# Performance work log

Hardware: AMD Instinct MI355X
Metric: run time of the kernel (lower is better)

The kernel has to match this reference:

```python
import jax, jax.numpy as jnp
import numpy as np
import math

HIDDEN = 1024
NUM_HEADS = 16
HEAD_DIM = 64
NUM_PREV = 4
BATCH = 4
SEQ = 1024
ROPE_BASE = 10000.0


def _rope(x):
    """Apply rotary embedding to x [..., seq, head_dim] (rotate-half form)."""
    d = x.shape[-1]
    s = x.shape[-2]
    inv_freq = 1.0 / (ROPE_BASE ** (jnp.arange(0, d, 2, dtype=jnp.float32) / d))
    ang = jnp.arange(s, dtype=jnp.float32)[:, None] * inv_freq[None, :]  # [s, d/2]
    cos, sin = jnp.cos(ang), jnp.sin(ang)
    x1, x2 = jnp.split(x, 2, axis=-1)
    return jnp.concatenate([x1 * cos - x2 * sin, x1 * sin + x2 * cos], axis=-1)


def setup_inputs() -> dict:
    key = jax.random.key(0)
    ks = jax.random.split(key, 8)
    std = 0.02
    d = {
        "hidden_states": jax.random.normal(ks[0], (BATCH, SEQ, HIDDEN), jnp.float32),
        "prev_hidden_states": jax.random.normal(ks[1], (NUM_PREV, BATCH, SEQ, HIDDEN), jnp.float32),
        "wq": jax.random.normal(ks[2], (HIDDEN, NUM_HEADS * HEAD_DIM), jnp.float32) * std,
        "bq": jnp.zeros((NUM_HEADS * HEAD_DIM,), jnp.float32),
        "wk": jax.random.normal(ks[3], (HIDDEN, NUM_HEADS * HEAD_DIM), jnp.float32) * std,
        "bk": jnp.zeros((NUM_HEADS * HEAD_DIM,), jnp.float32),
        "wv": jax.random.normal(ks[4], (HIDDEN, NUM_HEADS * HEAD_DIM), jnp.float32) * std,
        "bv": jnp.zeros((NUM_HEADS * HEAD_DIM,), jnp.float32),
        "wo": jax.random.normal(ks[5], (NUM_HEADS * HEAD_DIM, HIDDEN), jnp.float32) * std,
        "bo": jnp.zeros((HIDDEN,), jnp.float32),
        "wg": jax.random.normal(ks[6], (HIDDEN, NUM_PREV), jnp.float32) * std,
    }
    return d


def reference(hidden_states, prev_hidden_states, wq, bq, wk, bk, wv, bv, wo, bo, wg):
    B, S, H = hidden_states.shape
    P = prev_hidden_states.shape[0]
    nh, hd = NUM_HEADS, HEAD_DIM

    # Q projection + split heads + RoPE: [b, h, s, d]
    q = (hidden_states @ wq + bq).reshape(B, S, nh, hd).transpose(0, 2, 1, 3)
    q = _rope(q)

    # K/V projections for all prev layers at once: [p, b, h, s, d]
    k = (jnp.einsum('pbsh,he->pbse', prev_hidden_states, wk) + bk)
    k = k.reshape(P, B, S, nh, hd).transpose(0, 1, 3, 2, 4)
    k = _rope(k)
    v = (jnp.einsum('pbsh,he->pbse', prev_hidden_states, wv) + bv)
    v = v.reshape(P, B, S, nh, hd).transpose(0, 1, 3, 2, 4)

    # Attention per prev layer
    scale = 1.0 / math.sqrt(hd)
    attn = jnp.einsum('bhqd,pbhkd->pbhqk', q, k) * scale
    attn = jax.nn.softmax(attn, axis=-1)
    out = jnp.einsum('pbhqk,pbhkd->pbhqd', attn, v)  # [p, b, h, s, d]
    out = out.transpose(0, 1, 3, 2, 4).reshape(P, B, S, H)

    # Learned layer gating (faithful to original broadcast: requires B == P)
    pooled = jnp.mean(hidden_states, axis=1)            # [b, hidden]
    layer_w = jax.nn.softmax(pooled @ wg, axis=-1)      # [b, p]
    combined = jnp.sum(out * layer_w[:, :, None, None], axis=0)  # [b, s, hidden]

    return combined @ wo + bo
```

## Files before the change

kernel.cpp:

```cpp
#include <hip/hip_runtime.h>
#include <hip/hip_bf16.h>

#define B_  4
#define S_  1024
#define H_  1024
#define NH  16
#define HD  64
#define P_  4

typedef __attribute__((ext_vector_type(8))) short bf16x8;
typedef __attribute__((ext_vector_type(4))) float f32x4;
typedef __attribute__((ext_vector_type(16))) float f32x16;
typedef __attribute__((ext_vector_type(4))) unsigned int u32x4;

__device__ __forceinline__ float b2f(short s) {
  union { unsigned int u; float f; } v;
  v.u = ((unsigned int)(unsigned short)s) << 16;
  return v.f;
}
__device__ __forceinline__ short f2b(float f) {
  __hip_bfloat16 h = __float2bfloat16(f);
  return *reinterpret_cast<short*>(&h);
}
__device__ __forceinline__ float fast_exp2(float x) {
  float r;
  asm volatile("v_exp_f32 %0, %1" : "=v"(r) : "v"(x));
  return r;
}
__device__ __forceinline__ void gload_lds16(const void* g, void* l) {
  __builtin_amdgcn_global_load_lds(
      (const __attribute__((address_space(1))) unsigned int*)((uintptr_t)g),
      (__attribute__((address_space(3))) unsigned int*)((uintptr_t)l),
      16, 0, 0);
}

__global__ void prep_kernel(const float* __restrict__ hidden, const float* __restrict__ prev,
                            const float* __restrict__ wq, const float* __restrict__ wk,
                            const float* __restrict__ wv, const float* __restrict__ wo,
                            short* __restrict__ hbf, short* __restrict__ pbf,
                            short* __restrict__ wqT, short* __restrict__ wkT,
                            short* __restrict__ wvT, short* __restrict__ woT,
                            float* __restrict__ cost, float* __restrict__ sint,
                            float* __restrict__ pooled) {
  __shared__ short tile[32][33];
  int bid = blockIdx.x, tid = threadIdx.x;
  if (bid < 10240) {
    const float* src; short* dst; int idx;
    if (bid < 2048) { src = hidden; dst = hbf; idx = bid * 256 + tid; }
    else            { src = prev;   dst = pbf; idx = (bid - 2048) * 256 + tid; }
    const float4* s4 = (const float4*)(src + (size_t)idx * 8);
    float4 a = s4[0], b = s4[1];
    bf16x8 pk;
    pk[0] = f2b(a.x); pk[1] = f2b(a.y); pk[2] = f2b(a.z); pk[3] = f2b(a.w);
    pk[4] = f2b(b.x); pk[5] = f2b(b.y); pk[6] = f2b(b.z); pk[7] = f2b(b.w);
    *(bf16x8*)(dst + (size_t)idx * 8) = pk;
  } else if (bid < 14336) {
    int tb = bid - 10240;
    int z = tb >> 10, t = tb & 1023;
    const float* src = (z == 0) ? wq : (z == 1) ? wk : (z == 2) ? wv : wo;
    short*       dst = (z == 0) ? wqT : (z == 1) ? wkT : (z == 2) ? wvT : woT;
    int tx = tid & 31, ty = tid >> 5;
    int c0 = (t & 31) * 32, r0 = (t >> 5) * 32;
#pragma unroll
    for (int i = 0; i < 4; ++i)
      tile[ty + 8 * i][tx] = f2b(src[(r0 + ty + 8 * i) * 1024 + c0 + tx]);
    __syncthreads();
#pragma unroll
    for (int i = 0; i < 4; ++i)
      dst[(c0 + ty + 8 * i) * 1024 + r0 + tx] = tile[tx][ty + 8 * i];
  } else if (bid < 14464) {
    int idx = (bid - 14336) * 256 + tid;
    int s = idx >> 5, i = idx & 31;
    float invf = expf(-(float)i * (logf(10000.0f) / 32.0f));
    float a = (float)s * invf;
    cost[idx] = cosf(a);
    sint[idx] = sinf(a);
  } else {
    int idx = bid - 14464;
    int b = idx >> 5, chunk = idx & 31;
    const float* hp = hidden + (size_t)b * S_ * H_ + (size_t)chunk * 32 * H_ + tid * 4;
    float4 s = {0.f, 0.f, 0.f, 0.f};
#pragma unroll 4
    for (int t = 0; t < 32; ++t) {
      float4 v = *(const float4*)(hp + (size_t)t * H_);
      s.x += v.x; s.y += v.y; s.z += v.z; s.w += v.w;
    }
    float4 r;
    r.x = s.x * (1.0f / 1024.0f); r.y = s.y * (1.0f / 1024.0f);
    r.z = s.z * (1.0f / 1024.0f); r.w = s.w * (1.0f / 1024.0f);
    *(float4*)(pooled + (size_t)(b * 32 + chunk) * 1024 + tid * 4) = r;
  }
}

__global__ void gate_kernel(const float* __restrict__ pooled, const float* __restrict__ wg,
                            float* __restrict__ lw) {
  __shared__ float red[4][4];
  int b = blockIdx.x, tid = threadIdx.x;
  int w = tid >> 6, lane = tid & 63;
  int e0 = tid * 4;
  float4 pv = {0.f, 0.f, 0.f, 0.f};
#pragma unroll 4
  for (int ch = 0; ch < 32; ++ch) {
    float4 v = *(const float4*)&pooled[(size_t)(b * 32 + ch) * 1024 + e0];
    pv.x += v.x; pv.y += v.y; pv.z += v.z; pv.w += v.w;
  }
  float a[4];
#pragma unroll
  for (int j = 0; j < 4; ++j)
    a[j] = pv.x * wg[(e0 + 0) * 4 + j] + pv.y * wg[(e0 + 1) * 4 + j] +
           pv.z * wg[(e0 + 2) * 4 + j] + pv.w * wg[(e0 + 3) * 4 + j];
#pragma unroll
  for (int off = 32; off > 0; off >>= 1)
#pragma unroll
    for (int j = 0; j < 4; ++j) a[j] += __shfl_xor(a[j], off, 64);
  if (lane == 0) {
    red[w][0] = a[0]; red[w][1] = a[1]; red[w][2] = a[2]; red[w][3] = a[3];
  }
  __syncthreads();
  if (tid == 0) {
    float s0 = red[0][0] + red[1][0] + red[2][0] + red[3][0];
    float s1 = red[0][1] + red[1][1] + red[2][1] + red[3][1];
    float s2 = red[0][2] + red[1][2] + red[2][2] + red[3][2];
    float s3 = red[0][3] + red[1][3] + red[2][3] + red[3][3];
    float mx = fmaxf(fmaxf(s0, s1), fmaxf(s2, s3));
    float e0_ = expf(s0 - mx), e1 = expf(s1 - mx), e2 = expf(s2 - mx), e3 = expf(s3 - mx);
    float inv = 1.0f / (e0_ + e1 + e2 + e3);
    lw[b * 4 + 0] = e0_ * inv;
    lw[b * 4 + 1] = e1 * inv;
    lw[b * 4 + 2] = e2 * inv;
    lw[b * 4 + 3] = e3 * inv;
  }
}

__device__ __forceinline__ void rope_epilogue(const f32x4 (&acc)[4][4], const float* __restrict__ bias,
                                              short* __restrict__ outp,
                                              const float* __restrict__ cost,
                                              const float* __restrict__ sint,
                                              int m0, int wm, int quad, int c, int hh) {
  float b0 = bias[hh * 64 + c];
  float b1 = bias[hh * 64 + 16 + c];
  float b2_ = bias[hh * 64 + 32 + c];
  float b3 = bias[hh * 64 + 48 + c];
#pragma unroll
  for (int mt = 0; mt < 4; ++mt) {
    int gm = m0 + wm * 64 + mt * 16 + quad * 4;
#pragma unroll
    for (int j = 0; j < 4; ++j) {
      int m = gm + j;
      int s = m & 1023;
      int bbx = m >> 10;
      int orow = ((bbx * NH + hh) * S_ + s) * HD;
      float c0f = cost[s * 32 + c], s0f = sint[s * 32 + c];
      float x1 = acc[mt][0][j] + b0, x2 = acc[mt][2][j] + b2_;
      outp[orow + c]      = f2b(x1 * c0f - x2 * s0f);
      outp[orow + 32 + c] = f2b(x1 * s0f + x2 * c0f);
      float c1f = cost[s * 32 + 16 + c], s1f = sint[s * 32 + 16 + c];
      float y1 = acc[mt][1][j] + b1, y2 = acc[mt][3][j] + b3;
      outp[orow + 16 + c] = f2b(y1 * c1f - y2 * s1f);
      outp[orow + 48 + c] = f2b(y1 * s1f + y2 * c1f);
    }
  }
}

__launch_bounds__(256, 2)
__global__ void qkv_gemm(const short* __restrict__ hbf, const short* __restrict__ pbf,
                         const short* __restrict__ BTq, const short* __restrict__ BTk,
                         const short* __restrict__ BTv,
                         const float* __restrict__ bq, const float* __restrict__ bk,
                         const float* __restrict__ bv,
                         short* __restrict__ outq, short* __restrict__ outk,
                         short* __restrict__ outv,
                         const float* __restrict__ cost, const float* __restrict__ sint) {
  __shared__ __align__(16) short As[128 * 64];
  __shared__ __align__(16) short Bs1[128 * 64];
  __shared__ __align__(16) short Bs2[128 * 64];
  int id = blockIdx.x;
  int xcd = id & 7;
  int local = id >> 3;
  int n0i = local & 7;
  int yl = local >> 3;
  int y = yl * 8 + xcd;
  int tid = threadIdx.x;
  int lane = tid & 63, wvv = tid >> 6;
  int quad = lane >> 4, c = lane & 15;
  int wm = wvv & 1, wn = wvv >> 1;
  bool isQ = y < 32;
  int m0 = (isQ ? y : (y - 32)) * 128;
  int n0 = n0i * 128;
  const short* A  = isQ ? hbf : pbf;
  const short* B1 = isQ ? BTq : BTk;
  f32x4 acc1[4][4] = {}, acc2[4][4] = {};
  const short* Ab = A + (size_t)m0 * 1024;
  const short* Bb1 = B1 + (size_t)n0 * 1024;
  const short* Bb2 = BTv + (size_t)n0 * 1024;
  int sr = tid >> 3, sch = tid & 7;

  for (int kb = 0; kb < 16; ++kb) {
    int k0 = kb * 64;
    __syncthreads();
#pragma unroll
    for (int rd = 0; rd < 4; ++rd) {
      int row = sr + rd * 32;
      int col = ((sch ^ (row & 7)) * 8) + k0;
      gload_lds16(Ab + row * 1024 + col,  As  + rd * 2048 + tid * 8);
      gload_lds16(Bb1 + row * 1024 + col, Bs1 + rd * 2048 + tid * 8);
      if (!isQ) gload_lds16(Bb2 + row * 1024 + col, Bs2 + rd * 2048 + tid * 8);
    }
    __syncthreads();
#pragma unroll
    for (int ko = 0; ko < 2; ++ko) {
      bf16x8 af[4], b1f[4];
#pragma unroll
      for (int mt = 0; mt < 4; ++mt) {
        int row = wm * 64 + mt * 16 + c;
        af[mt] = *(const bf16x8*)&As[row * 64 + (((ko * 4 + quad) ^ (row & 7)) * 8)];
      }
#pragma unroll
      for (int nt = 0; nt < 4; ++nt) {
        int row = wn * 64 + nt * 16 + c;
        b1f[nt] = *(const bf16x8*)&Bs1[row * 64 + (((ko * 4 + quad) ^ (row & 7)) * 8)];
      }
#pragma unroll
      for (int mt = 0; mt < 4; ++mt)
#pragma unroll
        for (int nt = 0; nt < 4; ++nt)
          acc1[mt][nt] = __builtin_amdgcn_mfma_f32_16x16x32_bf16(af[mt], b1f[nt], acc1[mt][nt], 0, 0, 0);
      if (!isQ) {
        bf16x8 b2f_[4];
#pragma unroll
        for (int nt = 0; nt < 4; ++nt) {
          int row = wn * 64 + nt * 16 + c;
          b2f_[nt] = *(const bf16x8*)&Bs2[row * 64 + (((ko * 4 + quad) ^ (row & 7)) * 8)];
        }
#pragma unroll
        for (int mt = 0; mt < 4; ++mt)
#pragma unroll
          for (int nt = 0; nt < 4; ++nt)
            acc2[mt][nt] = __builtin_amdgcn_mfma_f32_16x16x32_bf16(af[mt], b2f_[nt], acc2[mt][nt], 0, 0, 0);
      }
    }
  }

  int colb = n0 + wn * 64;
  int hh = colb >> 6;
  if (isQ) {
    rope_epilogue(acc1, bq, outq, cost, sint, m0, wm, quad, c, hh);
  } else {
    rope_epilogue(acc1, bk, outk, cost, sint, m0, wm, quad, c, hh);
    float bb[4];
#pragma unroll
    for (int nt = 0; nt < 4; ++nt) bb[nt] = bv[hh * 64 + nt * 16 + c];
#pragma unroll
    for (int mt = 0; mt < 4; ++mt) {
      int gm = m0 + wm * 64 + mt * 16 + quad * 4;
      int s4 = gm & 1023, pb = gm >> 10;
#pragma unroll
      for (int nt = 0; nt < 4; ++nt) {
        int d = nt * 16 + c;
        ushort4 pk;
        pk.x = (unsigned short)f2b(acc2[mt][nt][0] + bb[nt]);
        pk.y = (unsigned short)f2b(acc2[mt][nt][1] + bb[nt]);
        pk.z = (unsigned short)f2b(acc2[mt][nt][2] + bb[nt]);
        pk.w = (unsigned short)f2b(acc2[mt][nt][3] + bb[nt]);
        *(ushort4*)&outv[((pb * NH + hh) * HD + d) * S_ + s4] = pk;
      }
    }
  }
}

__launch_bounds__(256, 2)
__global__ void attn_kernel(const short* __restrict__ q, const short* __restrict__ k,
                            const short* __restrict__ vt, const float* __restrict__ lw,
                            short* __restrict__ comb) {
  int blk = blockIdx.x;
  int x = blk & 7, qt = (blk >> 3) & 7, g = blk >> 6;
  int bh = g * 8 + x;
  int b = bh >> 4, h = bh & 15;
  int tid = threadIdx.x;
  int w = tid >> 6, lane = tid & 63;
  int l31 = lane & 31, hh = lane >> 5;
  int r7 = l31 & 7;

  __shared__ __align__(16) short Klds[2][64 * 64];
  __shared__ __align__(16) short Vlds[2][64 * 64];
  __shared__ float lsumf[4][32];

  const short* qbase = q + ((size_t)(b * NH + h) * S_ + qt * 128 + w * 32 + l31) * HD + hh * 8;
  bf16x8 aq[4];
#pragma unroll
  for (int st4 = 0; st4 < 4; ++st4) aq[st4] = *(const bf16x8*)(qbase + st4 * 16);

  float wl0 = lw[b], wl1 = lw[4 + b], wl2 = lw[8 + b], wl3 = lw[12 + b];

  const short* kbase = k + (size_t)(b * 16 + h) * S_ * HD;
  const short* vbase = vt + (size_t)(b * 16 + h) * HD * S_;
  const size_t pstr = (size_t)64 * S_ * HD;

  f32x16 C0 = {}, C1 = {};
  const float cs = 0.18033688011f;

  int sr = tid >> 3;
  int lc = (tid & 7) ^ (sr & 7);

#define STAGE_KV(kb2, vb2, kt2, bufi) do {                                 \
    const short* ksrc = (kb2) + ((kt2) * 64 + sr) * HD + lc * 8;           \
    gload_lds16(ksrc,           &Klds[bufi][tid * 8]);                     \
    gload_lds16(ksrc + 32 * HD, &Klds[bufi][2048 + tid * 8]);              \
    const short* vsrc = (vb2) + (size_t)sr * S_ + (kt2) * 64 + lc * 8;     \
    gload_lds16(vsrc,           &Vlds[bufi][tid * 8]);                     \
    gload_lds16(vsrc + 32 * S_, &Vlds[bufi][2048 + tid * 8]);              \
  } while (0)

  STAGE_KV(kbase, vbase, 0, 0);

#pragma unroll 1
  for (int p = 0; p < 4; ++p) {
    f32x16 O0 = {}, O1 = {};
    float ls0 = 0.f, ls1 = 0.f, ls2 = 0.f, ls3 = 0.f;

#pragma unroll 1
    for (int kt = 0; kt < 16; ++kt) {
      int t = p * 16 + kt;
      int cb = t & 1;
      if (t < 63) {
        int t1 = t + 1;
        int p2 = t1 >> 4, kt2 = t1 & 15;
        const short* kb2 = kbase + (size_t)p2 * pstr;
        const short* vb2 = vbase + (size_t)p2 * pstr;
        STAGE_KV(kb2, vb2, kt2, cb ^ 1);
        asm volatile("s_waitcnt vmcnt(4)" ::: "memory");
      } else {
        asm volatile("s_waitcnt vmcnt(0)" ::: "memory");
      }
      __builtin_amdgcn_s_barrier();
      __builtin_amdgcn_sched_barrier(0);

      u32x4 pa[4];
#pragma unroll
      for (int tau = 0; tau < 2; ++tau) {
        f32x16 st = {};
#pragma unroll
        for (int step = 0; step < 4; ++step) {
          bf16x8 kf = *(const bf16x8*)&Klds[cb][(tau * 32 + l31) * 64 + (((step * 2 + hh) ^ r7) * 8)];
          st = __builtin_amdgcn_mfma_f32_32x32x16_bf16(kf, aq[step], st, 0, 0, 0);
        }
        unsigned wb[8];
#pragma unroll
        for (int m = 0; m < 8; ++m) {
          float p0 = fast_exp2(st[2 * m] * cs);
          float p1 = fast_exp2(st[2 * m + 1] * cs);
          float ps = p0 + p1;
          if ((m & 3) == 0) ls0 += ps;
          else if ((m & 3) == 1) ls1 += ps;
          else if ((m & 3) == 2) ls2 += ps;
          else ls3 += ps;
          asm("v_cvt_pk_bf16_f32 %0, %1, %2" : "=v"(wb[m]) : "v"(p0), "v"(p1));
        }
#pragma unroll
        for (int gg = 0; gg < 2; ++gg) {
          unsigned x0 = wb[4 * gg + 0], y0 = wb[4 * gg + 2];
          unsigned x1 = wb[4 * gg + 1], y1 = wb[4 * gg + 3];
          asm volatile("v_permlane32_swap_b32 %0, %1" : "+v"(x0), "+v"(y0));
          asm volatile("v_permlane32_swap_b32 %0, %1" : "+v"(x1), "+v"(y1));
          u32x4 paw;
          paw[0] = x0; paw[1] = x1; paw[2] = y0; paw[3] = y1;
          pa[2 * tau + gg] = paw;
        }
      }

#pragma unroll
      for (int T = 0; T < 4; ++T) {
        bf16x8 ap = __builtin_bit_cast(bf16x8, pa[T]);
        bf16x8 vf0 = *(const bf16x8*)&Vlds[cb][l31 * 64 + (((T * 2 + hh) ^ r7) * 8)];
        O0 = __builtin_amdgcn_mfma_f32_32x32x16_bf16(ap, vf0, O0, 0, 0, 0);
        bf16x8 vf1 = *(const bf16x8*)&Vlds[cb][(32 + l31) * 64 + (((T * 2 + hh) ^ r7) * 8)];
        O1 = __builtin_amdgcn_mfma_f32_32x32x16_bf16(ap, vf1, O1, 0, 0, 0);
      }

      __builtin_amdgcn_s_barrier();
    }

    float lsum = (ls0 + ls1) + (ls2 + ls3);
    lsum += __shfl_xor(lsum, 32, 64);
    if (lane < 32) lsumf[w][l31] = lsum;
    float wl = (p == 0) ? wl0 : (p == 1) ? wl1 : (p == 2) ? wl2 : wl3;
#pragma unroll
    for (int gg = 0; gg < 4; ++gg) {
      f32x4 lv = *(const f32x4*)&lsumf[w][4 * hh + 8 * gg];
#pragma unroll
      for (int j = 0; j < 4; ++j) {
        float sc = wl / lv[j];
        C0[4 * gg + j] += O0[4 * gg + j] * sc;
        C1[4 * gg + j] += O1[4 * gg + j] * sc;
      }
    }
  }
#undef STAGE_KV

  short* ob = comb + ((size_t)b * S_ + qt * 128 + w * 32) * H_ + h * 64;
#pragma unroll
  for (int gg = 0; gg < 4; ++gg) {
#pragma unroll
    for (int j = 0; j < 4; ++j) {
      int qrow = 4 * hh + 8 * gg + j;
      ob[(size_t)qrow * H_ + l31]      = f2b(C0[4 * gg + j]);
      ob[(size_t)qrow * H_ + 32 + l31] = f2b(C1[4 * gg + j]);
    }
  }
}

__launch_bounds__(256, 4)
__global__ void gemm_out(const short* __restrict__ A, const short* __restrict__ BT,
                         const float* __restrict__ bias, float* __restrict__ outf) {
  __shared__ __align__(16) short As[64 * 64];
  __shared__ __align__(16) short Bs[128 * 64];
  int id = blockIdx.x;
  int xcd = id & 7;
  int local = id >> 3;
  int n0i = local & 7;
  int yl = local >> 3;
  int y = yl * 8 + xcd;
  int tid = threadIdx.x;
  int lane = tid & 63, wvv = tid >> 6;
  int quad = lane >> 4, c = lane & 15;
  int wm = wvv & 1, wn = wvv >> 1;
  int m0 = y * 64, n0 = n0i * 128;
  f32x4 acc[2][4] = {};
  const short* Ab = A + (size_t)m0 * 1024;
  const short* Bb = BT + (size_t)n0 * 1024;
  int sr = tid >> 3, sch = tid & 7;

  for (int kb = 0; kb < 16; ++kb) {
    int k0 = kb * 64;
    __syncthreads();
#pragma unroll
    for (int rd = 0; rd < 2; ++rd) {
      int row = sr + rd * 32;
      int col = ((sch ^ (row & 7)) * 8) + k0;
      gload_lds16(Ab + row * 1024 + col, As + rd * 2048 + tid * 8);
    }
#pragma unroll
    for (int rd = 0; rd < 4; ++rd) {
      int row = sr + rd * 32;
      int col = ((sch ^ (row & 7)) * 8) + k0;
      gload_lds16(Bb + row * 1024 + col, Bs + rd * 2048 + tid * 8);
    }
    __syncthreads();
#pragma unroll
    for (int ko = 0; ko < 2; ++ko) {
      bf16x8 af[2], bfr[4];
#pragma unroll
      for (int mt = 0; mt < 2; ++mt) {
        int row = wm * 32 + mt * 16 + c;
        af[mt] = *(const bf16x8*)&As[row * 64 + (((ko * 4 + quad) ^ (row & 7)) * 8)];
      }
#pragma unroll
      for (int nt = 0; nt < 4; ++nt) {
        int row = wn * 64 + nt * 16 + c;
        bfr[nt] = *(const bf16x8*)&Bs[row * 64 + (((ko * 4 + quad) ^ (row & 7)) * 8)];
      }
#pragma unroll
      for (int mt = 0; mt < 2; ++mt)
#pragma unroll
        for (int nt = 0; nt < 4; ++nt)
          acc[mt][nt] = __builtin_amdgcn_mfma_f32_16x16x32_bf16(af[mt], bfr[nt], acc[mt][nt], 0, 0, 0);
    }
  }

  int colb = n0 + wn * 64;
  float bb[4];
#pragma unroll
  for (int nt = 0; nt < 4; ++nt) bb[nt] = bias[colb + nt * 16 + c];
#pragma unroll
  for (int mt = 0; mt < 2; ++mt) {
    int gm = m0 + wm * 32 + mt * 16 + quad * 4;
#pragma unroll
    for (int j = 0; j < 4; ++j) {
      int m = gm + j;
#pragma unroll
      for (int nt = 0; nt < 4; ++nt)
        outf[(size_t)m * 1024 + colb + nt * 16 + c] = acc[mt][nt][j] + bb[nt];
    }
  }
}

extern "C" void kernel_launch(void* const* d_in, const int* in_sizes, int n_in,
                              void* d_out, int out_size, void* d_ws, size_t ws_size,
                              hipStream_t stream) {
  (void)in_sizes; (void)n_in; (void)out_size; (void)ws_size;
  const float* hidden = (const float*)d_in[0];
  const float* prev   = (const float*)d_in[1];
  const float* wq = (const float*)d_in[2];
  const float* bq = (const float*)d_in[3];
  const float* wk = (const float*)d_in[4];
  const float* bk = (const float*)d_in[5];
  const float* wv = (const float*)d_in[6];
  const float* bv = (const float*)d_in[7];
  const float* wo = (const float*)d_in[8];
  const float* bo = (const float*)d_in[9];
  const float* wg = (const float*)d_in[10];
  float* out = (float*)d_out;
  char* ws = (char*)d_ws;

  size_t off = 0;
  short* wqT = (short*)(ws + off); off += (size_t)1024 * 1024 * 2;
  short* wkT = (short*)(ws + off); off += (size_t)1024 * 1024 * 2;
  short* wvT = (short*)(ws + off); off += (size_t)1024 * 1024 * 2;
  short* woT = (short*)(ws + off); off += (size_t)1024 * 1024 * 2;
  short* hbf = (short*)(ws + off); off += (size_t)B_ * S_ * H_ * 2;
  short* pbf = (short*)(ws + off); off += (size_t)P_ * B_ * S_ * H_ * 2;
  short* qbf = (short*)(ws + off); off += (size_t)B_ * S_ * H_ * 2;
  short* kbf = (short*)(ws + off); off += (size_t)P_ * B_ * S_ * H_ * 2;
  short* vtb = (short*)(ws + off); off += (size_t)P_ * B_ * S_ * H_ * 2;
  float* cost = (float*)(ws + off); off += (size_t)S_ * 32 * 4;
  float* sint = (float*)(ws + off); off += (size_t)S_ * 32 * 4;
  float* pooled = (float*)(ws + off); off += (size_t)B_ * 32 * 1024 * 4;
  float* lw = (float*)(ws + off); off += 64;
  short* comb = pbf;

  prep_kernel<<<14592, 256, 0, stream>>>(hidden, prev, wq, wk, wv, wo,
                                         hbf, pbf, wqT, wkT, wvT, woT,
                                         cost, sint, pooled);
  gate_kernel<<<4, 256, 0, stream>>>(pooled, wg, lw);
  qkv_gemm<<<1280, 256, 0, stream>>>(hbf, pbf, wqT, wkT, wvT,
                                     bq, bk, bv, qbf, kbf, vtb, cost, sint);
  attn_kernel<<<512, 256, 0, stream>>>(qbf, kbf, vtb, lw, comb);
  gemm_out<<<512, 256, 0, stream>>>(comb, woT, bo, out);
}
```

Baseline: 332.7 us.

## Split attention over prev-layer pairs and sum partials in output GEMM

The attention grid doubles from 512 to 1024 blocks. Each block now handles two of the four previous layers instead of all four and writes a gated partial result into one of two buffers. The output GEMM loads both partial buffers, adds them in fp32 and rounds to bf16 before the LDS store, replacing the async global-to-LDS copy for A. Launch bounds rise to 4 blocks per CU. The aim is more parallelism and occupancy for attention, at the cost of extra A traffic, synchronous loads in the GEMM and an extra bf16 rounding.

```diff
diff --git a/kernel.cpp b/kernel.cpp
--- a/kernel.cpp
+++ b/kernel.cpp
@@ -268,12 +268,15 @@
   }
 }
 
-__launch_bounds__(256, 2)
+__launch_bounds__(256, 4)
 __global__ void attn_kernel(const short* __restrict__ q, const short* __restrict__ k,
                             const short* __restrict__ vt, const float* __restrict__ lw,
-                            short* __restrict__ comb) {
+                            short* __restrict__ combA, short* __restrict__ combB) {
   int blk = blockIdx.x;
-  int x = blk & 7, qt = (blk >> 3) & 7, g = blk >> 6;
+  int x = blk & 7;
+  int pp = (blk >> 3) & 1;
+  int qt = (blk >> 4) & 7;
+  int g = blk >> 7;
   int bh = g * 8 + x;
   int b = bh >> 4, h = bh & 15;
   int tid = threadIdx.x;
@@ -290,10 +293,11 @@
 #pragma unroll
   for (int st4 = 0; st4 < 4; ++st4) aq[st4] = *(const bf16x8*)(qbase + st4 * 16);
 
-  float wl0 = lw[b], wl1 = lw[4 + b], wl2 = lw[8 + b], wl3 = lw[12 + b];
-
-  const short* kbase = k + (size_t)(b * 16 + h) * S_ * HD;
-  const short* vbase = vt + (size_t)(b * 16 + h) * HD * S_;
+  float wla = lw[(pp * 2 + 0) * 4 + b];
+  float wlb = lw[(pp * 2 + 1) * 4 + b];
+
+  const short* kbase = k + (size_t)((pp * 2) * 64 + b * 16 + h) * S_ * HD;
+  const short* vbase = vt + (size_t)((pp * 2) * 64 + b * 16 + h) * HD * S_;
   const size_t pstr = (size_t)64 * S_ * HD;
 
   f32x16 C0 = {}, C1 = {};
@@ -314,15 +318,15 @@
   STAGE_KV(kbase, vbase, 0, 0);
 
 #pragma unroll 1
-  for (int p = 0; p < 4; ++p) {
+  for (int pl = 0; pl < 2; ++pl) {
     f32x16 O0 = {}, O1 = {};
     float ls0 = 0.f, ls1 = 0.f, ls2 = 0.f, ls3 = 0.f;
 
 #pragma unroll 1
     for (int kt = 0; kt < 16; ++kt) {
-      int t = p * 16 + kt;
+      int t = pl * 16 + kt;
       int cb = t & 1;
-      if (t < 63) {
+      if (t < 31) {
         int t1 = t + 1;
         int p2 = t1 >> 4, kt2 = t1 & 15;
         const short* kb2 = kbase + (size_t)p2 * pstr;
@@ -383,7 +387,7 @@
     float lsum = (ls0 + ls1) + (ls2 + ls3);
     lsum += __shfl_xor(lsum, 32, 64);
     if (lane < 32) lsumf[w][l31] = lsum;
-    float wl = (p == 0) ? wl0 : (p == 1) ? wl1 : (p == 2) ? wl2 : wl3;
+    float wl = (pl == 0) ? wla : wlb;
 #pragma unroll
     for (int gg = 0; gg < 4; ++gg) {
       f32x4 lv = *(const f32x4*)&lsumf[w][4 * hh + 8 * gg];
@@ -397,7 +401,8 @@
   }
 #undef STAGE_KV
 
-  short* ob = comb + ((size_t)b * S_ + qt * 128 + w * 32) * H_ + h * 64;
+  short* cp = pp ? combB : combA;
+  short* ob = cp + ((size_t)b * S_ + qt * 128 + w * 32) * H_ + h * 64;
 #pragma unroll
   for (int gg = 0; gg < 4; ++gg) {
 #pragma unroll
@@ -410,7 +415,8 @@
 }
 
 __launch_bounds__(256, 4)
-__global__ void gemm_out(const short* __restrict__ A, const short* __restrict__ BT,
+__global__ void gemm_out(const short* __restrict__ A0, const short* __restrict__ A1,
+                         const short* __restrict__ BT,
                          const float* __restrict__ bias, float* __restrict__ outf) {
   __shared__ __align__(16) short As[64 * 64];
   __shared__ __align__(16) short Bs[128 * 64];
@@ -426,7 +432,8 @@
   int wm = wvv & 1, wn = wvv >> 1;
   int m0 = y * 64, n0 = n0i * 128;
   f32x4 acc[2][4] = {};
-  const short* Ab = A + (size_t)m0 * 1024;
+  const short* Ab0 = A0 + (size_t)m0 * 1024;
+  const short* Ab1 = A1 + (size_t)m0 * 1024;
   const short* Bb = BT + (size_t)n0 * 1024;
   int sr = tid >> 3, sch = tid & 7;
 
@@ -437,7 +444,12 @@
     for (int rd = 0; rd < 2; ++rd) {
       int row = sr + rd * 32;
       int col = ((sch ^ (row & 7)) * 8) + k0;
-      gload_lds16(Ab + row * 1024 + col, As + rd * 2048 + tid * 8);
+      bf16x8 va = *(const bf16x8*)(Ab0 + (size_t)row * 1024 + col);
+      bf16x8 vb = *(const bf16x8*)(Ab1 + (size_t)row * 1024 + col);
+      bf16x8 vs;
+#pragma unroll
+      for (int j = 0; j < 8; ++j) vs[j] = f2b(b2f(va[j]) + b2f(vb[j]));
+      *(bf16x8*)(As + rd * 2048 + tid * 8) = vs;
     }
 #pragma unroll
     for (int rd = 0; rd < 4; ++rd) {
@@ -516,7 +528,8 @@
   float* sint = (float*)(ws + off); off += (size_t)S_ * 32 * 4;
   float* pooled = (float*)(ws + off); off += (size_t)B_ * 32 * 1024 * 4;
   float* lw = (float*)(ws + off); off += 64;
-  short* comb = pbf;
+  short* combA = pbf;
+  short* combB = hbf;
 
   prep_kernel<<<14592, 256, 0, stream>>>(hidden, prev, wq, wk, wv, wo,
                                          hbf, pbf, wqT, wkT, wvT, woT,
@@ -524,6 +537,6 @@
   gate_kernel<<<4, 256, 0, stream>>>(pooled, wg, lw);
   qkv_gemm<<<1280, 256, 0, stream>>>(hbf, pbf, wqT, wkT, wvT,
                                      bq, bk, bv, qbf, kbf, vtb, cost, sint);
-  attn_kernel<<<512, 256, 0, stream>>>(qbf, kbf, vtb, lw, comb);
-  gemm_out<<<512, 256, 0, stream>>>(comb, woT, bo, out);
-}
+  attn_kernel<<<1024, 256, 0, stream>>>(qbf, kbf, vtb, lw, combA, combB);
+  gemm_out<<<512, 256, 0, stream>>>(combA, combB, woT, bo, out);
+}
```

Measured after the change: 359.6 us. 1.08x slower.
